# Kernel tuning notes

Hardware: AMD Instinct MI355X
Metric: run time of the kernel (lower is better)

## Reference

```python
import jax, jax.numpy as jnp
import numpy as np
import itertools

NUM_HEADS = 8
KEY_DIM = 32
ATTN_D = 128  # attn_ratio * key_dim
BN_EPS = 1e-5


def _build_idxs(rx=16, rz=8, tn=1):
    points = list(itertools.product(range(rx), range(rx)))
    for i in range(tn):
        points += list(itertools.product(range(rx + rz * i, rx + rz * (i + 1)),
                                         range(rx + rz * i, rx + rz * (i + 1))))
    offsets = {}
    idxs = []
    for p1 in points:
        for p2 in points:
            off = (abs(p1[0] - p2[0]), abs(p1[1] - p2[1]))
            if off not in offsets:
                offsets[off] = len(offsets)
            idxs.append(offsets[off])
    N = len(points)
    return np.asarray(idxs, dtype=np.int64).reshape(N, N), len(offsets)


def _bn_train(x2d, gamma, beta):
    # BatchNorm1d in training mode: batch mean / biased variance over dim 0
    m = jnp.mean(x2d, axis=0)
    v = jnp.var(x2d, axis=0)
    return (x2d - m) * jax.lax.rsqrt(v + BN_EPS) * gamma + beta


def setup_inputs() -> dict:
    key = jax.random.key(0)
    ks = jax.random.split(key, 4)
    idxs_np, n_off = _build_idxs()  # (320,320), 560
    B, N, C = 128, idxs_np.shape[0], 256
    h = NUM_HEADS * (2 * KEY_DIM + ATTN_D)  # 1536
    dh = NUM_HEADS * ATTN_D  # 1024
    return {
        "x": jax.random.normal(ks[0], (B, N, C), dtype=jnp.float32),
        "Wqkv": jax.random.normal(ks[1], (h, C), dtype=jnp.float32) * 0.02,
        "g1": jnp.ones((h,), jnp.float32),
        "b1": jnp.zeros((h,), jnp.float32),
        "ab": jax.random.normal(ks[2], (NUM_HEADS, n_off), dtype=jnp.float32) * 0.02,
        "Wproj": jax.random.normal(ks[3], (C, dh), dtype=jnp.float32) * 0.02,
        "g2": jnp.ones((C,), jnp.float32),
        "b2": jnp.zeros((C,), jnp.float32),
        "idxs": jnp.asarray(idxs_np),
    }


def reference(x, Wqkv, g1, b1, ab, Wproj, g2, b2, idxs):
    B, N, C = x.shape
    scale = KEY_DIM ** -0.5
    # qkv projection (Linear no-bias) + BatchNorm1d over flattened (B*N, h)
    qkv = jnp.einsum('bnc,hc->bnh', x, Wqkv)
    qkv = _bn_train(qkv.reshape(B * N, -1), g1, b1).reshape(B, N, NUM_HEADS, 2 * KEY_DIM + ATTN_D)
    q = qkv[..., :KEY_DIM]
    k = qkv[..., KEY_DIM:2 * KEY_DIM]
    v = qkv[..., 2 * KEY_DIM:]
    bias = ab[:, idxs]  # gather -> (H, N, N)
    attn = jnp.einsum('bnhd,bmhd->bhnm', q, k) * scale + bias[None]
    attn = jax.nn.softmax(attn, axis=-1)
    out = jnp.einsum('bhnm,bmhd->bnhd', attn, v).reshape(B, N, NUM_HEADS * ATTN_D)
    out = jax.nn.gelu(out, approximate=False)  # activation() before proj
    out = jnp.einsum('bnd,cd->bnc', out, Wproj)
    out = _bn_train(out.reshape(B * N, -1), g2, b2).reshape(B, N, C)
    return out
```

## Files before the change

### kernel.cpp

```cpp
#include <hip/hip_runtime.h>
#include <hip/hip_bf16.h>

#define B_ 128
#define N_ 320
#define C_ 256
#define H_ 8
#define HQKV 1536
#define DH 1024
#define MROWS 40960
#define EPS 1e-5f
#define SCALE 0.17677669529663687f
#define LOG2E 1.4426950408889634f

typedef __attribute__((ext_vector_type(4))) float f32x4;
typedef __attribute__((ext_vector_type(8))) short short8_t;
typedef __attribute__((ext_vector_type(4))) short short4_t;
typedef __attribute__((ext_vector_type(4))) unsigned short ushort4_t;

__device__ inline float bf2f(unsigned short u) { return __uint_as_float(((unsigned)u) << 16); }
__device__ inline unsigned short f2bf(float f) {
    unsigned u = __float_as_uint(f);
    u += 0x7FFF + ((u >> 16) & 1);
    return (unsigned short)(u >> 16);
}

__device__ inline float gelu_f(float v) {
    float v2 = v * v;
    float w = fmaf(v2, 0.044715f, 1.0f);
    float z = v * w * (-2.3022098f);
    float e = __builtin_amdgcn_exp2f(z);
    return v * __builtin_amdgcn_rcpf(1.0f + e);
}

#define GLD16(gp, lp)                                                                  \
    __builtin_amdgcn_global_load_lds((const __attribute__((address_space(1))) void*)(gp), \
                                     (__attribute__((address_space(3))) void*)(lp), 16, 0, 0)

__global__ void conv_all(const float* __restrict__ x, const float* __restrict__ wqkv,
                         const float* __restrict__ wproj, unsigned short* __restrict__ xb,
                         unsigned short* __restrict__ wqb, unsigned short* __restrict__ wpb) {
    int i = blockIdx.x * 256 + threadIdx.x;
    const float* src;
    unsigned short* dst;
    int off;
    if (i < 2621440) { src = x; dst = xb; off = i; }
    else if (i < 2719744) { src = wqkv; dst = wqb; off = i - 2621440; }
    else if (i < 2785280) { src = wproj; dst = wpb; off = i - 2719744; }
    else return;
    f32x4 v = ((const f32x4*)src)[off];
    short4_t o;
#pragma unroll
    for (int j = 0; j < 4; ++j) o[j] = (short)f2bf(v[j]);
    ((short4_t*)dst)[off] = o;
}

__global__ __launch_bounds__(256) void gemm_qkv(const unsigned short* __restrict__ A,
                                                const unsigned short* __restrict__ Bm,
                                                unsigned short* __restrict__ qkB,
                                                unsigned short* __restrict__ vT,
                                                float* __restrict__ sum1, float* __restrict__ sumsq1) {
    __shared__ unsigned short lA[2][128 * 32];
    __shared__ unsigned short lB[2][128 * 32];
    const int tid = threadIdx.x;
    const int lane = tid & 63, wid = tid >> 6;
    const int wm = wid >> 1, wn = wid & 1;
    const int lr = lane & 15, g = lane >> 4, lk = g * 8;
    const int orig = blockIdx.y * 12 + blockIdx.x;
    const int id2 = (orig & 7) * 480 + (orig >> 3);
    const int m0 = (id2 / 12) * 128, n0 = (id2 % 12) * 128;
    const int wb0 = tid & 192;
    const int srow = tid >> 2, scg = (tid & 3) * 8;

#define STAGE_QKV(it, buf)                                                               \
    {                                                                                    \
        int k0 = (it) * 32;                                                              \
        GLD16(&A[(size_t)(m0 + srow) * 256 + k0 + scg], &lA[buf][(size_t)wb0 * 8]);      \
        GLD16(&Bm[(size_t)(n0 + srow) * 256 + k0 + scg], &lB[buf][(size_t)wb0 * 8]);     \
        GLD16(&A[(size_t)(m0 + 64 + srow) * 256 + k0 + scg], &lA[buf][2048 + (size_t)wb0 * 8]); \
        GLD16(&Bm[(size_t)(n0 + 64 + srow) * 256 + k0 + scg], &lB[buf][2048 + (size_t)wb0 * 8]); \
    }

    STAGE_QKV(0, 0);
    f32x4 acc[4][4] = {};
    for (int it = 0; it < 8; ++it) {
        __syncthreads();
        if (it < 7) STAGE_QKV(it + 1, (it + 1) & 1);
        const unsigned short* la = lA[it & 1];
        const unsigned short* lb = lB[it & 1];
        short8_t af[4], bfr[4];
#pragma unroll
        for (int i = 0; i < 4; ++i) af[i] = *(const short8_t*)&la[(wm * 64 + i * 16 + lr) * 32 + lk];
#pragma unroll
        for (int j = 0; j < 4; ++j) bfr[j] = *(const short8_t*)&lb[(wn * 64 + j * 16 + lr) * 32 + lk];
#pragma unroll
        for (int i = 0; i < 4; ++i)
#pragma unroll
            for (int j = 0; j < 4; ++j)
                acc[i][j] = __builtin_amdgcn_mfma_f32_16x16x32_bf16(af[i], bfr[j], acc[i][j], 0, 0, 0);
    }
    int hhj[4], cmj[4];
#pragma unroll
    for (int j = 0; j < 4; ++j) {
        int col = n0 + wn * 64 + j * 16 + lr;
        hhj[j] = col / 192;
        cmj[j] = col - hhj[j] * 192;
    }
    float cs[4] = {0.f, 0.f, 0.f, 0.f}, css[4] = {0.f, 0.f, 0.f, 0.f};
#pragma unroll
    for (int i = 0; i < 4; ++i) {
        int rowbase = m0 + wm * 64 + i * 16 + g * 4;
        int bq = rowbase / 320;
        int n = rowbase - bq * 320;
#pragma unroll
        for (int j = 0; j < 4; ++j) {
            float v0 = acc[i][j][0], v1 = acc[i][j][1], v2 = acc[i][j][2], v3 = acc[i][j][3];
            cs[j] += (v0 + v1) + (v2 + v3);
            css[j] += (v0 * v0 + v1 * v1) + (v2 * v2 + v3 * v3);
            if (cmj[j] < 64) {
                unsigned short* qp = &qkB[((size_t)(bq * 8 + hhj[j]) * 320 + n) * 64 + cmj[j]];
                qp[0] = f2bf(v0); qp[64] = f2bf(v1); qp[128] = f2bf(v2); qp[192] = f2bf(v3);
            } else {
                short4_t o;
                o[0] = (short)f2bf(v0); o[1] = (short)f2bf(v1);
                o[2] = (short)f2bf(v2); o[3] = (short)f2bf(v3);
                *(short4_t*)&vT[((size_t)(bq * 8 + hhj[j]) * 128 + (cmj[j] - 64)) * 320 + n] = o;
            }
        }
    }
    __syncthreads();
    float* red_s = (float*)lA;
    float* red_ss = (float*)lB;
#pragma unroll
    for (int j = 0; j < 4; ++j) {
        int c = wn * 64 + j * 16 + lr;
        red_s[(wm * 4 + g) * 128 + c] = cs[j];
        red_ss[(wm * 4 + g) * 128 + c] = css[j];
    }
    __syncthreads();
    if (tid < 128) {
        float s = 0.f;
#pragma unroll
        for (int u = 0; u < 8; ++u) s += red_s[u * 128 + tid];
        atomicAdd(&sum1[n0 + tid], s);
    } else {
        int c = tid - 128;
        float s = 0.f;
#pragma unroll
        for (int u = 0; u < 8; ++u) s += red_ss[u * 128 + c];
        atomicAdd(&sumsq1[n0 + c], s);
    }
}

__global__ __launch_bounds__(256) void gemm_proj(const unsigned short* __restrict__ A,
                                                 const unsigned short* __restrict__ Bm,
                                                 float* __restrict__ Cout,
                                                 float* __restrict__ sum2, float* __restrict__ sumsq2) {
    __shared__ unsigned short lA[2][64 * 32];
    __shared__ unsigned short lB[2][128 * 32];
    const int tid = threadIdx.x;
    const int lane = tid & 63, wid = tid >> 6;
    const int wm = wid >> 1, wn = wid & 1;
    const int lr = lane & 15, g = lane >> 4, lk = g * 8;
    const int m0 = blockIdx.y * 64, n0 = blockIdx.x * 128;
    const int wb0 = tid & 192;
    const int srow = tid >> 2, scg = (tid & 3) * 8;

#define STAGE_PROJ(it, buf)                                                              \
    {                                                                                    \
        int k0 = (it) * 32;                                                              \
        GLD16(&A[(size_t)(m0 + srow) * 1024 + k0 + scg], &lA[buf][(size_t)wb0 * 8]);     \
        GLD16(&Bm[(size_t)(n0 + srow) * 1024 + k0 + scg], &lB[buf][(size_t)wb0 * 8]);    \
        GLD16(&Bm[(size_t)(n0 + 64 + srow) * 1024 + k0 + scg], &lB[buf][2048 + (size_t)wb0 * 8]); \
    }

    STAGE_PROJ(0, 0);
    f32x4 acc[2][4] = {};
    for (int it = 0; it < 32; ++it) {
        __syncthreads();
        if (it < 31) STAGE_PROJ(it + 1, (it + 1) & 1);
        const unsigned short* la = lA[it & 1];
        const unsigned short* lb = lB[it & 1];
        short8_t af[2], bfr[4];
#pragma unroll
        for (int i = 0; i < 2; ++i) af[i] = *(const short8_t*)&la[(wm * 32 + i * 16 + lr) * 32 + lk];
#pragma unroll
        for (int j = 0; j < 4; ++j) bfr[j] = *(const short8_t*)&lb[(wn * 64 + j * 16 + lr) * 32 + lk];
#pragma unroll
        for (int i = 0; i < 2; ++i)
#pragma unroll
            for (int j = 0; j < 4; ++j)
                acc[i][j] = __builtin_amdgcn_mfma_f32_16x16x32_bf16(af[i], bfr[j], acc[i][j], 0, 0, 0);
    }
    float cs[4] = {0.f, 0.f, 0.f, 0.f}, css[4] = {0.f, 0.f, 0.f, 0.f};
#pragma unroll
    for (int i = 0; i < 2; ++i) {
#pragma unroll
        for (int r = 0; r < 4; ++r) {
            int row = m0 + wm * 32 + i * 16 + g * 4 + r;
#pragma unroll
            for (int j = 0; j < 4; ++j) {
                float val = acc[i][j][r];
                cs[j] += val;
                css[j] += val * val;
                Cout[(size_t)row * 256 + n0 + wn * 64 + j * 16 + lr] = val;
            }
        }
    }
    __syncthreads();
    float* red_s = (float*)lB;
    float* red_ss = (float*)lB + 1024;
#pragma unroll
    for (int j = 0; j < 4; ++j) {
        int c = wn * 64 + j * 16 + lr;
        red_s[(wm * 4 + g) * 128 + c] = cs[j];
        red_ss[(wm * 4 + g) * 128 + c] = css[j];
    }
    __syncthreads();
    if (tid < 128) {
        float s = 0.f;
#pragma unroll
        for (int u = 0; u < 8; ++u) s += red_s[u * 128 + tid];
        atomicAdd(&sum2[n0 + tid], s);
    } else {
        int c = tid - 128;
        float s = 0.f;
#pragma unroll
        for (int u = 0; u < 8; ++u) s += red_ss[u * 128 + c];
        atomicAdd(&sumsq2[n0 + c], s);
    }
}

__global__ void bn_finalize(const float* __restrict__ sum, const float* __restrict__ sumsq,
                            const float* __restrict__ g, const float* __restrict__ b,
                            float* __restrict__ scale, float* __restrict__ shift, int C, float invM) {
    int c = blockIdx.x * 256 + threadIdx.x;
    if (c < C) {
        float mean = sum[c] * invM;
        float var = sumsq[c] * invM - mean * mean;
        float sc = g[c] * rsqrtf(var + EPS);
        scale[c] = sc;
        shift[c] = b[c] - mean * sc;
    }
}

__global__ void uk_kernel(const unsigned short* __restrict__ qkB, const float* __restrict__ scale1,
                          const float* __restrict__ shift1, float* __restrict__ uk) {
    __shared__ float w2l[256];
    {
        int c = threadIdx.x;
        int hh = c >> 5, cc = c & 31;
        int qch = hh * 192 + cc;
        w2l[c] = shift1[qch] * scale1[qch + 32] * (SCALE * LOG2E);
    }
    __syncthreads();
    int idx = blockIdx.x * 256 + threadIdx.x;
    if (idx < 128 * 8 * 320) {
        int bh = idx / 320;
        int h = bh & 7;
        const unsigned short* kp = &qkB[(size_t)idx * 64 + 32];
        float s = 0.f;
#pragma unroll
        for (int c4 = 0; c4 < 4; ++c4) {
            short8_t kk = *(const short8_t*)&kp[c4 * 8];
#pragma unroll
            for (int j = 0; j < 8; ++j) s += bf2f((unsigned short)kk[j]) * w2l[(h << 5) + c4 * 8 + j];
        }
        uk[idx] = s;
    }
}

__global__ void bias_build(const float* __restrict__ ab, const int* __restrict__ idxs,
                           unsigned short* __restrict__ biasb, int n_off) {
    int i = blockIdx.x * 256 + threadIdx.x;
    if (i < H_ * N_ * N_) {
        int r = i & 3;
        int m = (i >> 2) % 320;
        int nq = ((i >> 2) / 320) % 80;
        int h = i / 102400;
        int n = nq * 4 + r;
        biasb[i] = f2bf(ab[h * n_off + idxs[n * 320 + m]] * LOG2E);
    }
}

__global__ __launch_bounds__(256, 4) void attn_kernel(const unsigned short* __restrict__ qkB,
                                                      const unsigned short* __restrict__ vT,
                                                      const float* __restrict__ uk,
                                                      const unsigned short* __restrict__ biasb,
                                                      const float* __restrict__ scale1,
                                                      const float* __restrict__ shift1,
                                                      unsigned short* __restrict__ attnout) {
    __shared__ unsigned short Plds[4][10][16][40];
    __shared__ float sums[64];
    const int tid = threadIdx.x;
    const int lane = tid & 63, wid = tid >> 6;
    const int lr = lane & 15, g = lane >> 4;
    const int h = blockIdx.x;
    const int b = blockIdx.y / 5, qt = blockIdx.y % 5;
    const int bh = b * 8 + h;

    int qrow = qt * 64 + wid * 16 + lr;
    short8_t qraw = *(const short8_t*)&qkB[((size_t)bh * 320 + qrow) * 64 + g * 8];
    short8_t aq;
    const int cq = h * 192 + g * 8;
#pragma unroll
    for (int j = 0; j < 8; ++j) {
        float w = scale1[cq + j] * scale1[cq + 32 + j] * (SCALE * LOG2E);
        aq[j] = (short)f2bf(bf2f((unsigned short)qraw[j]) * w);
    }

    const unsigned short* Kbase = &qkB[(size_t)bh * 320 * 64 + 32 + g * 8];
    f32x4 sacc[20];
    __builtin_amdgcn_s_setprio(1);
#pragma unroll
    for (int t = 0; t < 20; ++t) {
        short8_t bk = *(const short8_t*)&Kbase[(size_t)(t * 16 + lr) * 64];
        f32x4 z = {};
        sacc[t] = __builtin_amdgcn_mfma_f32_16x16x32_bf16(aq, bk, z, 0, 0, 0);
    }
    __builtin_amdgcn_s_setprio(0);

    const int nloc0 = qt * 64 + wid * 16 + g * 4;
    const unsigned short* biasrow = &biasb[((size_t)h * 80 + (nloc0 >> 2)) * 1280];
    const float* ukrow = &uk[(size_t)bh * 320];
    float sumr[4] = {0.f, 0.f, 0.f, 0.f};
#pragma unroll
    for (int t = 0; t < 20; ++t) {
        float ukv = ukrow[t * 16 + lr];
        ushort4_t b4 = *(const ushort4_t*)&biasrow[(t * 16 + lr) * 4];
#pragma unroll
        for (int r = 0; r < 4; ++r) {
            float s = sacc[t][r] + ukv + bf2f(b4[r]);
            float p = __builtin_amdgcn_exp2f(s);
            sumr[r] += p;
            Plds[wid][t >> 1][g * 4 + r][(t & 1) * 16 + lr] = f2bf(p);
        }
    }
#pragma unroll
    for (int r = 0; r < 4; ++r) {
#pragma unroll
        for (int ms = 1; ms < 16; ms <<= 1) sumr[r] += __shfl_xor(sumr[r], ms);
        if (lr == 0) sums[wid * 16 + g * 4 + r] = sumr[r];
    }
    __syncthreads();

    const unsigned short* Vb = &vT[(size_t)bh * 128 * 320 + g * 8];
    f32x4 oacc[4][2] = {};
    __builtin_amdgcn_s_setprio(1);
#pragma unroll
    for (int t = 0; t < 10; ++t) {
        short8_t bv0 = *(const short8_t*)&Vb[(size_t)(wid * 32 + lr) * 320 + t * 32];
        short8_t bv1 = *(const short8_t*)&Vb[(size_t)(wid * 32 + 16 + lr) * 320 + t * 32];
#pragma unroll
        for (int qw = 0; qw < 4; ++qw) {
            short8_t ap = *(short8_t*)&Plds[qw][t][lr][g * 8];
            oacc[qw][0] = __builtin_amdgcn_mfma_f32_16x16x32_bf16(ap, bv0, oacc[qw][0], 0, 0, 0);
            oacc[qw][1] = __builtin_amdgcn_mfma_f32_16x16x32_bf16(ap, bv1, oacc[qw][1], 0, 0, 0);
        }
    }
    __builtin_amdgcn_s_setprio(0);

    float svv[2], tvv[2];
#pragma unroll
    for (int dtl = 0; dtl < 2; ++dtl) {
        int ch = h * 192 + 64 + wid * 32 + dtl * 16 + lr;
        svv[dtl] = scale1[ch];
        tvv[dtl] = shift1[ch];
    }
#pragma unroll
    for (int qw = 0; qw < 4; ++qw) {
#pragma unroll
        for (int r = 0; r < 4; ++r) {
            float inv = __builtin_amdgcn_rcpf(sums[qw * 16 + g * 4 + r]);
            size_t nrow = (size_t)b * 320 + qt * 64 + qw * 16 + g * 4 + r;
#pragma unroll
            for (int dtl = 0; dtl < 2; ++dtl) {
                float v = oacc[qw][dtl][r] * inv * svv[dtl] + tvv[dtl];
                attnout[nrow * 1024 + h * 128 + wid * 32 + dtl * 16 + lr] = f2bf(gelu_f(v));
            }
        }
    }
}

__global__ void bn_apply(float* __restrict__ out, const float* __restrict__ sum2,
                         const float* __restrict__ sumsq2, const float* __restrict__ g2,
                         const float* __restrict__ b2) {
    __shared__ float sc[256], sh[256];
    {
        int c = threadIdx.x;
        float mean = sum2[c] * (1.0f / MROWS);
        float var = sumsq2[c] * (1.0f / MROWS) - mean * mean;
        float s = g2[c] * rsqrtf(var + EPS);
        sc[c] = s;
        sh[c] = b2[c] - mean * s;
    }
    __syncthreads();
    int i = blockIdx.x * 256 + threadIdx.x;
    const int total = MROWS * C_ / 4;
    for (; i < total; i += gridDim.x * 256) {
        f32x4 v = *(const f32x4*)&out[(size_t)i * 4];
        int c = (i * 4) & 255;
        f32x4 o;
#pragma unroll
        for (int j = 0; j < 4; ++j) o[j] = v[j] * sc[c + j] + sh[c + j];
        *(f32x4*)&out[(size_t)i * 4] = o;
    }
}

extern "C" void kernel_launch(void* const* d_in, const int* in_sizes, int n_in,
                              void* d_out, int out_size, void* d_ws, size_t ws_size,
                              hipStream_t stream) {
    const float* x = (const float*)d_in[0];
    const float* Wqkv = (const float*)d_in[1];
    const float* g1 = (const float*)d_in[2];
    const float* b1 = (const float*)d_in[3];
    const float* ab = (const float*)d_in[4];
    const float* Wproj = (const float*)d_in[5];
    const float* g2 = (const float*)d_in[6];
    const float* b2 = (const float*)d_in[7];
    const int* idxs = (const int*)d_in[8];
    const int n_off = in_sizes[4] / H_;

    char* ws = (char*)d_ws;
    unsigned short* qkB = (unsigned short*)ws;
    unsigned short* vT = (unsigned short*)(ws + 41943040);
    unsigned short* attnout = (unsigned short*)(ws + 125829120);
    unsigned short* xb = attnout;
    unsigned short* biasb = (unsigned short*)(ws + 209715200);
    float* uk = (float*)(ws + 212992000);
    unsigned short* wqb = (unsigned short*)(ws + 214302720);
    unsigned short* wpb = (unsigned short*)(ws + 215089152);
    float* stats = (float*)(ws + 215613440);
    float* sum1 = stats;
    float* sumsq1 = stats + 1536;
    float* sum2 = stats + 3072;
    float* sumsq2 = sum2 + 256;
    float* scale1 = sumsq2 + 256;
    float* shift1 = scale1 + 1536;

    hipMemsetAsync(stats, 0, 3584 * 4, stream);
    conv_all<<<dim3(10880), 256, 0, stream>>>(x, Wqkv, Wproj, xb, wqb, wpb);
    bias_build<<<dim3(3200), 256, 0, stream>>>(ab, idxs, biasb, n_off);
    gemm_qkv<<<dim3(12, 320), 256, 0, stream>>>(xb, wqb, qkB, vT, sum1, sumsq1);
    bn_finalize<<<dim3(6), 256, 0, stream>>>(sum1, sumsq1, g1, b1, scale1, shift1, 1536, 1.0f / MROWS);
    uk_kernel<<<dim3(1280), 256, 0, stream>>>(qkB, scale1, shift1, uk);
    attn_kernel<<<dim3(8, 640), 256, 0, stream>>>(qkB, vT, uk, biasb, scale1, shift1, attnout);
    gemm_proj<<<dim3(2, 640), 256, 0, stream>>>(attnout, wpb, (float*)d_out, sum2, sumsq2);
    bn_apply<<<dim3(2048), 256, 0, stream>>>((float*)d_out, sum2, sumsq2, g2, b2);
}
```

Baseline: 287.1 us.

## Widen projection GEMM tile to full 256 output columns per block

The projection GEMM block now covers all 256 output columns for a 64-row slab, and each wave computes a 64x64 subtile instead of 32x64. The A operand (attention output) is therefore read from global memory once instead of twice, and the grid shrinks from 1280 blocks to 640. The BN statistics reduction is simplified to one pass per thread with two atomics. In exchange, LDS use and accumulator registers per thread grow, and a launch bound asking for 4 blocks per unit is added, which may cause register pressure or spills.

After: 285.7 us. Within noise of the previous version (-0.5%).

```diff
diff --git a/kernel.cpp b/kernel.cpp
--- a/kernel.cpp
+++ b/kernel.cpp
@@ -151,82 +151,87 @@
     }
 }
 
-__global__ __launch_bounds__(256) void gemm_proj(const unsigned short* __restrict__ A,
-                                                 const unsigned short* __restrict__ Bm,
-                                                 float* __restrict__ Cout,
-                                                 float* __restrict__ sum2, float* __restrict__ sumsq2) {
+__global__ __launch_bounds__(256, 4) void gemm_proj(const unsigned short* __restrict__ A,
+                                                    const unsigned short* __restrict__ Bm,
+                                                    float* __restrict__ Cout,
+                                                    float* __restrict__ sum2,
+                                                    float* __restrict__ sumsq2) {
     __shared__ unsigned short lA[2][64 * 32];
-    __shared__ unsigned short lB[2][128 * 32];
+    __shared__ unsigned short lB[2][256 * 32];
     const int tid = threadIdx.x;
     const int lane = tid & 63, wid = tid >> 6;
-    const int wm = wid >> 1, wn = wid & 1;
+    const int wn = wid;
     const int lr = lane & 15, g = lane >> 4, lk = g * 8;
-    const int m0 = blockIdx.y * 64, n0 = blockIdx.x * 128;
+    const int m0 = blockIdx.x * 64;
     const int wb0 = tid & 192;
-    const int srow = tid >> 2, scg = (tid & 3) * 8;
 
 #define STAGE_PROJ(it, buf)                                                              \
     {                                                                                    \
         int k0 = (it) * 32;                                                              \
-        GLD16(&A[(size_t)(m0 + srow) * 1024 + k0 + scg], &lA[buf][(size_t)wb0 * 8]);     \
-        GLD16(&Bm[(size_t)(n0 + srow) * 1024 + k0 + scg], &lB[buf][(size_t)wb0 * 8]);    \
-        GLD16(&Bm[(size_t)(n0 + 64 + srow) * 1024 + k0 + scg], &lB[buf][2048 + (size_t)wb0 * 8]); \
+        GLD16(&A[(size_t)(m0 + (tid >> 2)) * 1024 + k0 + (tid & 3) * 8],                 \
+              &lA[buf][(size_t)wb0 * 8]);                                                \
+        GLD16(&Bm[(size_t)(tid >> 2) * 1024 + k0 + (tid & 3) * 8],                       \
+              &lB[buf][(size_t)wb0 * 8]);                                                \
+        GLD16(&Bm[(size_t)(64 + (tid >> 2)) * 1024 + k0 + (tid & 3) * 8],                \
+              &lB[buf][2048 + (size_t)wb0 * 8]);                                         \
+        GLD16(&Bm[(size_t)(128 + (tid >> 2)) * 1024 + k0 + (tid & 3) * 8],               \
+              &lB[buf][4096 + (size_t)wb0 * 8]);                                         \
+        GLD16(&Bm[(size_t)(192 + (tid >> 2)) * 1024 + k0 + (tid & 3) * 8],               \
+              &lB[buf][6144 + (size_t)wb0 * 8]);                                         \
     }
 
     STAGE_PROJ(0, 0);
-    f32x4 acc[2][4] = {};
+    f32x4 acc[4][4] = {};
     for (int it = 0; it < 32; ++it) {
         __syncthreads();
         if (it < 31) STAGE_PROJ(it + 1, (it + 1) & 1);
         const unsigned short* la = lA[it & 1];
         const unsigned short* lb = lB[it & 1];
-        short8_t af[2], bfr[4];
-#pragma unroll
-        for (int i = 0; i < 2; ++i) af[i] = *(const short8_t*)&la[(wm * 32 + i * 16 + lr) * 32 + lk];
+        short8_t af[4], bfr[4];
+#pragma unroll
+        for (int i = 0; i < 4; ++i) af[i] = *(const short8_t*)&la[(i * 16 + lr) * 32 + lk];
 #pragma unroll
         for (int j = 0; j < 4; ++j) bfr[j] = *(const short8_t*)&lb[(wn * 64 + j * 16 + lr) * 32 + lk];
 #pragma unroll
-        for (int i = 0; i < 2; ++i)
+        for (int i = 0; i < 4; ++i)
 #pragma unroll
             for (int j = 0; j < 4; ++j)
                 acc[i][j] = __builtin_amdgcn_mfma_f32_16x16x32_bf16(af[i], bfr[j], acc[i][j], 0, 0, 0);
     }
     float cs[4] = {0.f, 0.f, 0.f, 0.f}, css[4] = {0.f, 0.f, 0.f, 0.f};
 #pragma unroll
-    for (int i = 0; i < 2; ++i) {
+    for (int i = 0; i < 4; ++i) {
 #pragma unroll
         for (int r = 0; r < 4; ++r) {
-            int row = m0 + wm * 32 + i * 16 + g * 4 + r;
+            int row = m0 + i * 16 + g * 4 + r;
 #pragma unroll
             for (int j = 0; j < 4; ++j) {
                 float val = acc[i][j][r];
                 cs[j] += val;
                 css[j] += val * val;
-                Cout[(size_t)row * 256 + n0 + wn * 64 + j * 16 + lr] = val;
+                Cout[(size_t)row * 256 + wn * 64 + j * 16 + lr] = val;
             }
         }
     }
     __syncthreads();
-    float* red_s = (float*)lB;
-    float* red_ss = (float*)lB + 1024;
+    float* red_s = (float*)lA;
+    float* red_ss = (float*)lB;
 #pragma unroll
     for (int j = 0; j < 4; ++j) {
         int c = wn * 64 + j * 16 + lr;
-        red_s[(wm * 4 + g) * 128 + c] = cs[j];
-        red_ss[(wm * 4 + g) * 128 + c] = css[j];
-    }
-    __syncthreads();
-    if (tid < 128) {
-        float s = 0.f;
-#pragma unroll
-        for (int u = 0; u < 8; ++u) s += red_s[u * 128 + tid];
-        atomicAdd(&sum2[n0 + tid], s);
-    } else {
-        int c = tid - 128;
-        float s = 0.f;
-#pragma unroll
-        for (int u = 0; u < 8; ++u) s += red_ss[u * 128 + c];
-        atomicAdd(&sumsq2[n0 + c], s);
+        red_s[g * 256 + c] = cs[j];
+        red_ss[g * 256 + c] = css[j];
+    }
+    __syncthreads();
+    {
+        float s = 0.f, ss = 0.f;
+#pragma unroll
+        for (int u = 0; u < 4; ++u) {
+            s += red_s[u * 256 + tid];
+            ss += red_ss[u * 256 + tid];
+        }
+        atomicAdd(&sum2[tid], s);
+        atomicAdd(&sumsq2[tid], ss);
     }
 }
 
@@ -444,6 +449,6 @@
     bn_finalize<<<dim3(6), 256, 0, stream>>>(sum1, sumsq1, g1, b1, scale1, shift1, 1536, 1.0f / MROWS);
     uk_kernel<<<dim3(1280), 256, 0, stream>>>(qkB, scale1, shift1, uk);
     attn_kernel<<<dim3(8, 640), 256, 0, stream>>>(qkB, vT, uk, biasb, scale1, shift1, attnout);
-    gemm_proj<<<dim3(2, 640), 256, 0, stream>>>(attnout, wpb, (float*)d_out, sum2, sumsq2);
+    gemm_proj<<<dim3(640), 256, 0, stream>>>(attnout, wpb, (float*)d_out, sum2, sumsq2);
     bn_apply<<<dim3(2048), 256, 0, stream>>>((float*)d_out, sum2, sumsq2, g2, b2);
 }
```
